# Kernel tuning notes

Hardware: AMD Instinct MI355X
Metric: run time of the kernel (lower is better)

Reference implementation:

```python
import jax, jax.numpy as jnp
import numpy as np

VOCAB, EMB, HID, B, T = 50000, 16, 32, 4096, 500


def setup_inputs() -> dict:
    key = jax.random.key(0)
    k1, k2, k3, k4 = jax.random.split(key, 4)
    tokens = jax.random.randint(k1, (B, T), 0, VOCAB, dtype=jnp.int32)
    emb_table = jax.random.normal(k2, (VOCAB, EMB), dtype=jnp.float32) * 0.05
    kernel = jax.random.normal(k3, (EMB, 4 * HID), dtype=jnp.float32) * (1.0 / np.sqrt(EMB))
    rec_kernel = jax.random.normal(k4, (HID, 4 * HID), dtype=jnp.float32) * (1.0 / np.sqrt(HID))
    # Keras default: unit_forget_bias=True -> forget-gate bias = 1
    bias = jnp.concatenate([
        jnp.zeros((HID,), jnp.float32),
        jnp.ones((HID,), jnp.float32),
        jnp.zeros((2 * HID,), jnp.float32),
    ])
    return {"tokens": tokens, "emb_table": emb_table, "kernel": kernel,
            "rec_kernel": rec_kernel, "bias": bias}


def reference(tokens, emb_table, kernel, rec_kernel, bias):
    # Embedding with mask_zero=True: mask = tokens != 0
    embedded = emb_table[tokens]                 # [B, T, EMB]
    mask = (tokens != 0)                         # [B, T] bool
    # Precompute input projections for all timesteps (one big GEMM)
    x_proj = jnp.einsum('bte,eh->bth', embedded, kernel) + bias  # [B, T, 4H]

    def step(carry, xs):
        h, c = carry                              # [B, H] each
        xp_t, m_t = xs                            # [B, 4H], [B]
        z = xp_t + h @ rec_kernel                 # [B, 4H]
        i, f, g, o = jnp.split(z, 4, axis=-1)     # Keras gate order i,f,c,o
        i = jax.nn.sigmoid(i)
        f = jax.nn.sigmoid(f)
        g = jnp.tanh(g)
        o = jax.nn.sigmoid(o)
        c_new = f * c + i * g
        h_new = o * jnp.tanh(c_new)
        m = m_t[:, None]
        # masked steps carry previous state through (Keras LSTM mask semantics)
        h = jnp.where(m, h_new, h)
        c = jnp.where(m, c_new, c)
        return (h, c), None

    h0 = jnp.zeros((tokens.shape[0], HID), jnp.float32)
    c0 = jnp.zeros((tokens.shape[0], HID), jnp.float32)
    xs = (jnp.swapaxes(x_proj, 0, 1), jnp.swapaxes(mask, 0, 1))  # time-major
    (h, c), _ = jax.lax.scan(step, (h0, c0), xs)
    return h                                      # [B, HID] last (masked) output
```

## Files before the change

### kernel.cpp

```cpp
#include <hip/hip_runtime.h>
#include <cstdint>

#define VOCAB_N 50000
#define EMB_N   16
#define HID_N   32
#define B_N     4096
#define T_N     500

static_assert((T_N & 1) == 0, "T must be even");

__device__ __forceinline__ float frcp(float x) { return __builtin_amdgcn_rcpf(x); }
__device__ __forceinline__ float sigm(float x) {
  return frcp(1.0f + exp2f(x * -1.44269504088896341f));
}
__device__ __forceinline__ float tanh_fast(float x) {
  float e = exp2f(x * 2.88539008177792681f);
  return fmaf(-2.0f, frcp(e + 1.0f), 1.0f);
}

__global__ void build_proj_kernel(const float* __restrict__ emb,
                                  const float* __restrict__ W,
                                  const float* __restrict__ bias,
                                  float* __restrict__ proj) {
  __shared__ float Wl[EMB_N * 128];
  __shared__ float bl[128];
  const int tid = threadIdx.x;
  for (int i = tid; i < EMB_N * 128 / 4; i += 256)
    reinterpret_cast<float4*>(Wl)[i] = reinterpret_cast<const float4*>(W)[i];
  if (tid < 32)
    reinterpret_cast<float4*>(bl)[tid] = reinterpret_cast<const float4*>(bias)[tid];
  __syncthreads();

  const int gtid = blockIdx.x * 256 + tid;
  const int v = gtid >> 5;
  const int j = gtid & 31;
  if (v >= VOCAB_N) return;

  const float4* ev = reinterpret_cast<const float4*>(emb + (size_t)v * EMB_N);
  float4 e0 = ev[0], e1 = ev[1], e2 = ev[2], e3 = ev[3];
  const float em[16] = {e0.x,e0.y,e0.z,e0.w, e1.x,e1.y,e1.z,e1.w,
                        e2.x,e2.y,e2.z,e2.w, e3.x,e3.y,e3.z,e3.w};
  float a0 = bl[j], a1 = bl[32+j], a2 = bl[64+j], a3 = bl[96+j];
#pragma unroll
  for (int e = 0; e < 16; ++e) {
    float x = em[e];
    a0 = fmaf(x, Wl[e*128      + j], a0);
    a1 = fmaf(x, Wl[e*128 + 32 + j], a1);
    a2 = fmaf(x, Wl[e*128 + 64 + j], a2);
    a3 = fmaf(x, Wl[e*128 + 96 + j], a3);
  }
  reinterpret_cast<float4*>(proj)[(size_t)v * 32 + j] = make_float4(a0, a1, a2, a3);
}

template<bool TABLE>
__global__ __launch_bounds__(256, 2)
void lstm_scan_kernel(const int*   __restrict__ tokens,
                      const float* __restrict__ rec_kernel,
                      const float* __restrict__ proj,
                      const float* __restrict__ emb,
                      const float* __restrict__ W,
                      const float* __restrict__ bias,
                      float*       __restrict__ out) {
  __shared__ int   tokl[8][T_N];
  __shared__ float hbuf[8][HID_N];

  const int tid  = threadIdx.x;
  const int wv   = tid >> 6;
  const int lane = tid & 63;
  const int half = lane >> 5;
  const int j    = lane & 31;
  const int wrow = wv * 2 + half;
  const int row  = blockIdx.x * 8 + wrow;

  {
    const int4* src = reinterpret_cast<const int4*>(tokens + (size_t)blockIdx.x * 8 * T_N);
    int4* dst = reinterpret_cast<int4*>(&tokl[0][0]);
    for (int i = tid; i < 8 * T_N / 4; i += 256) dst[i] = src[i];
  }

  float wr[HID_N][4];
#pragma unroll
  for (int k = 0; k < HID_N; ++k) {
#pragma unroll
    for (int g = 0; g < 4; ++g) wr[k][g] = rec_kernel[k * 128 + g * 32 + j];
  }

  float wk[EMB_N][4];
  float bb[4];
  if (!TABLE) {
#pragma unroll
    for (int e = 0; e < EMB_N; ++e) {
#pragma unroll
      for (int g = 0; g < 4; ++g) wk[e][g] = W[e * 128 + g * 32 + j];
    }
#pragma unroll
    for (int g = 0; g < 4; ++g) bb[g] = bias[g * 32 + j];
  }
  __syncthreads();

  float c = 0.0f, h = 0.0f;
  float4 h4[8];
#pragma unroll
  for (int q = 0; q < 8; ++q) h4[q] = make_float4(0.f, 0.f, 0.f, 0.f);

  int tokc  = tokl[wrow][0];
  int tokc1 = tokl[wrow][1];
  float4 pA = make_float4(0,0,0,0), pB = make_float4(0,0,0,0);
  float4 eA[4], eB[4];
  if (TABLE) {
    pA = reinterpret_cast<const float4*>(proj)[(size_t)tokc  * 32 + j];
    pB = reinterpret_cast<const float4*>(proj)[(size_t)tokc1 * 32 + j];
  } else {
#pragma unroll
    for (int q = 0; q < 4; ++q) eA[q] = reinterpret_cast<const float4*>(emb + (size_t)tokc  * EMB_N)[q];
#pragma unroll
    for (int q = 0; q < 4; ++q) eB[q] = reinterpret_cast<const float4*>(emb + (size_t)tokc1 * EMB_N)[q];
  }

  auto body = [&](int t, float4& p, float4* eb) {
    int tp = t + 2; if (tp >= T_N) tp = T_N - 1;
    const int tokp = tokl[wrow][tp];

    float a0, a1, a2, a3;
    if (TABLE) {
      a0 = p.x; a1 = p.y; a2 = p.z; a3 = p.w;
    } else {
      const float em[16] = {eb[0].x,eb[0].y,eb[0].z,eb[0].w, eb[1].x,eb[1].y,eb[1].z,eb[1].w,
                            eb[2].x,eb[2].y,eb[2].z,eb[2].w, eb[3].x,eb[3].y,eb[3].z,eb[3].w};
      a0 = bb[0]; a1 = bb[1]; a2 = bb[2]; a3 = bb[3];
#pragma unroll
      for (int e = 0; e < EMB_N; ++e) {
        float x = em[e];
        a0 = fmaf(x, wk[e][0], a0); a1 = fmaf(x, wk[e][1], a1);
        a2 = fmaf(x, wk[e][2], a2); a3 = fmaf(x, wk[e][3], a3);
      }
    }

#pragma unroll
    for (int q = 0; q < 8; ++q) {
      float hx = h4[q].x, hy = h4[q].y, hz = h4[q].z, hw = h4[q].w;
      a0 = fmaf(hx, wr[4*q+0][0], a0); a1 = fmaf(hx, wr[4*q+0][1], a1);
      a2 = fmaf(hx, wr[4*q+0][2], a2); a3 = fmaf(hx, wr[4*q+0][3], a3);
      a0 = fmaf(hy, wr[4*q+1][0], a0); a1 = fmaf(hy, wr[4*q+1][1], a1);
      a2 = fmaf(hy, wr[4*q+1][2], a2); a3 = fmaf(hy, wr[4*q+1][3], a3);
      a0 = fmaf(hz, wr[4*q+2][0], a0); a1 = fmaf(hz, wr[4*q+2][1], a1);
      a2 = fmaf(hz, wr[4*q+2][2], a2); a3 = fmaf(hz, wr[4*q+2][3], a3);
      a0 = fmaf(hw, wr[4*q+3][0], a0); a1 = fmaf(hw, wr[4*q+3][1], a1);
      a2 = fmaf(hw, wr[4*q+3][2], a2); a3 = fmaf(hw, wr[4*q+3][3], a3);
    }

    if (TABLE) {
      p = reinterpret_cast<const float4*>(proj)[(size_t)tokp * 32 + j];
    } else {
#pragma unroll
      for (int q = 0; q < 4; ++q)
        eb[q] = reinterpret_cast<const float4*>(emb + (size_t)tokp * EMB_N)[q];
    }

    float ig = sigm(a0);
    float fg = sigm(a1);
    float gg = tanh_fast(a2);
    float og = sigm(a3);
    float cn = fmaf(fg, c, ig * gg);
    float hn = og * tanh_fast(cn);
    if (tokc != 0) { h = hn; c = cn; }

    hbuf[wrow][j] = h;
    asm volatile("" ::: "memory");
#pragma unroll
    for (int q = 0; q < 8; ++q)
      h4[q] = reinterpret_cast<const float4*>(&hbuf[wrow][0])[q];
    asm volatile("" ::: "memory");

    tokc = tokc1;
    tokc1 = tokp;
  };

  for (int t = 0; t < T_N; t += 2) {
    body(t,     pA, eA);
    body(t + 1, pB, eB);
  }

  out[(size_t)row * HID_N + j] = h;
}

extern "C" void kernel_launch(void* const* d_in, const int* in_sizes, int n_in,
                              void* d_out, int out_size, void* d_ws, size_t ws_size,
                              hipStream_t stream) {
  const int*   tokens = (const int*)  d_in[0];
  const float* emb    = (const float*)d_in[1];
  const float* W      = (const float*)d_in[2];
  const float* rec    = (const float*)d_in[3];
  const float* bias   = (const float*)d_in[4];
  float* out = (float*)d_out;

  const size_t need = (size_t)VOCAB_N * 32 * 4 * sizeof(float);
  if (ws_size >= need) {
    float* proj = (float*)d_ws;
    build_proj_kernel<<<(VOCAB_N * 32) / 256, 256, 0, stream>>>(emb, W, bias, proj);
    lstm_scan_kernel<true><<<B_N / 8, 256, 0, stream>>>(tokens, rec, proj,
                                                        emb, W, bias, out);
  } else {
    lstm_scan_kernel<false><<<B_N / 8, 256, 0, stream>>>(tokens, rec, nullptr,
                                                         emb, W, bias, out);
  }
}
```

Before: 354.6 us.

## Spread each LSTM row across a full wavefront with two gates per lane

The scan kernel now maps one batch row to a 64-lane wavefront instead of half a wavefront, and each lane computes two gate pre-activations (i/g or f/o). Gates are exchanged with a cross-half shuffle. The projection table is relaid out as float2 per lane, and masked steps skip the gate math and the hidden-state LDS round trip. Token ids are made wave-uniform with readfirstlane, and occupancy bounds are raised. The aim is to halve the per-lane FMA chain on the serial recurrence, at the cost of more waves, shuffles and divergent-free branching overhead.

```diff
diff --git a/kernel.cpp b/kernel.cpp
--- a/kernel.cpp
+++ b/kernel.cpp
@@ -6,22 +6,14 @@
 #define HID_N   32
 #define B_N     4096
 #define T_N     500
-
-static_assert((T_N & 1) == 0, "T must be even");
+#define TPAD    512
 
 __device__ __forceinline__ float frcp(float x) { return __builtin_amdgcn_rcpf(x); }
-__device__ __forceinline__ float sigm(float x) {
-  return frcp(1.0f + exp2f(x * -1.44269504088896341f));
-}
-__device__ __forceinline__ float tanh_fast(float x) {
-  float e = exp2f(x * 2.88539008177792681f);
-  return fmaf(-2.0f, frcp(e + 1.0f), 1.0f);
-}
-
-__global__ void build_proj_kernel(const float* __restrict__ emb,
-                                  const float* __restrict__ W,
-                                  const float* __restrict__ bias,
-                                  float* __restrict__ proj) {
+
+__global__ void build_proj2_kernel(const float* __restrict__ emb,
+                                   const float* __restrict__ W,
+                                   const float* __restrict__ bias,
+                                   float2* __restrict__ proj2) {
   __shared__ float Wl[EMB_N * 128];
   __shared__ float bl[128];
   const int tid = threadIdx.x;
@@ -31,36 +23,167 @@
     reinterpret_cast<float4*>(bl)[tid] = reinterpret_cast<const float4*>(bias)[tid];
   __syncthreads();
 
-  const int gtid = blockIdx.x * 256 + tid;
-  const int v = gtid >> 5;
-  const int j = gtid & 31;
+  const int gid = blockIdx.x * 256 + tid;
+  const int v = gid >> 6;
+  const int l = gid & 63;
   if (v >= VOCAB_N) return;
 
   const float4* ev = reinterpret_cast<const float4*>(emb + (size_t)v * EMB_N);
   float4 e0 = ev[0], e1 = ev[1], e2 = ev[2], e3 = ev[3];
   const float em[16] = {e0.x,e0.y,e0.z,e0.w, e1.x,e1.y,e1.z,e1.w,
                         e2.x,e2.y,e2.z,e2.w, e3.x,e3.y,e3.z,e3.w};
-  float a0 = bl[j], a1 = bl[32+j], a2 = bl[64+j], a3 = bl[96+j];
-#pragma unroll
-  for (int e = 0; e < 16; ++e) {
-    float x = em[e];
-    a0 = fmaf(x, Wl[e*128      + j], a0);
-    a1 = fmaf(x, Wl[e*128 + 32 + j], a1);
-    a2 = fmaf(x, Wl[e*128 + 64 + j], a2);
-    a3 = fmaf(x, Wl[e*128 + 96 + j], a3);
-  }
-  reinterpret_cast<float4*>(proj)[(size_t)v * 32 + j] = make_float4(a0, a1, a2, a3);
-}
-
-template<bool TABLE>
+  float a0 = bl[l], a1 = bl[64 + l];
+#pragma unroll
+  for (int e = 0; e < EMB_N; ++e) {
+    a0 = fmaf(em[e], Wl[e * 128 + l],      a0);
+    a1 = fmaf(em[e], Wl[e * 128 + 64 + l], a1);
+  }
+  proj2[(size_t)v * 64 + l] = make_float2(a0, a1);
+}
+
+__global__ __launch_bounds__(256, 4)
+void lstm_scan2_kernel(const int*    __restrict__ tokens,
+                       const float*  __restrict__ rec_kernel,
+                       const float2* __restrict__ proj2,
+                       float*        __restrict__ out) {
+  __shared__ int   tokl[4][TPAD];
+  __shared__ float hbuf[4][HID_N];
+
+  const int tid  = threadIdx.x;
+  const int wrow = tid >> 6;
+  const int lane = tid & 63;
+  const int l    = lane;
+  const int row  = blockIdx.x * 4 + wrow;
+
+  {
+    const int4* src = reinterpret_cast<const int4*>(tokens + (size_t)blockIdx.x * 4 * T_N);
+    for (int i = tid; i < 4 * T_N / 4; i += 256) {
+      int4 v4 = src[i];
+      int g = 4 * i;
+      int r = g / T_N;
+      int cidx = g - r * T_N;
+      *reinterpret_cast<int4*>(&tokl[r][cidx]) = v4;
+    }
+    if (tid < 48) {
+      int r = tid / 12, cc = T_N + (tid % 12);
+      tokl[r][cc] = 0;
+    }
+  }
+
+  float wr0[HID_N], wr1[HID_N];
+#pragma unroll
+  for (int k = 0; k < HID_N; ++k) {
+    wr0[k] = rec_kernel[k * 128 + l];
+    wr1[k] = rec_kernel[k * 128 + 64 + l];
+  }
+
+  const bool lo = (lane < 32);
+  const float sB = lo ?  2.8853900817779268f : -1.4426950408889634f;
+  const float mB = lo ? -2.0f : 1.0f;
+  const float aB = lo ?  1.0f : 0.0f;
+
+  __syncthreads();
+
+  float c = 0.0f, h = 0.0f;
+  float4 h4[8];
+#pragma unroll
+  for (int q = 0; q < 8; ++q) h4[q] = make_float4(0.f, 0.f, 0.f, 0.f);
+
+  float* hrow = &hbuf[wrow][0];
+  const int kidx = lane & 31;
+
+  int4 g0v = *reinterpret_cast<const int4*>(&tokl[wrow][0]);
+  int4 g1v = *reinterpret_cast<const int4*>(&tokl[wrow][4]);
+  int tg0 = __builtin_amdgcn_readfirstlane(g0v.x);
+  int tg1 = __builtin_amdgcn_readfirstlane(g0v.y);
+  int tg2 = __builtin_amdgcn_readfirstlane(g0v.z);
+  int tg3 = __builtin_amdgcn_readfirstlane(g0v.w);
+  int tn0 = __builtin_amdgcn_readfirstlane(g1v.x);
+  int tn1 = __builtin_amdgcn_readfirstlane(g1v.y);
+  int tn2 = __builtin_amdgcn_readfirstlane(g1v.z);
+  int tn3 = __builtin_amdgcn_readfirstlane(g1v.w);
+
+  float2 p0 = proj2[(size_t)tg0 * 64 + l];
+  float2 p1 = proj2[(size_t)tg1 * 64 + l];
+
+  auto step = [&](int stok, int ptok, float2& pcur) {
+    const float xA = pcur.x, xB = pcur.y;
+
+    pcur = proj2[(size_t)ptok * 64 + l];
+
+    float a0 = xA, a1 = xB, b0 = 0.f, b1 = 0.f;
+#pragma unroll
+    for (int q = 0; q < 8; ++q) {
+      const float4 hq = h4[q];
+      a0 = fmaf(hq.x, wr0[4*q+0], a0); a1 = fmaf(hq.x, wr1[4*q+0], a1);
+      b0 = fmaf(hq.y, wr0[4*q+1], b0); b1 = fmaf(hq.y, wr1[4*q+1], b1);
+      a0 = fmaf(hq.z, wr0[4*q+2], a0); a1 = fmaf(hq.z, wr1[4*q+2], a1);
+      b0 = fmaf(hq.w, wr0[4*q+3], b0); b1 = fmaf(hq.w, wr1[4*q+3], b1);
+    }
+    const float zA = a0 + b0;
+    const float zB = a1 + b1;
+
+    if (stok != 0) {
+      float eA = exp2f(zA * -1.4426950408889634f);
+      float P  = frcp(1.0f + eA);
+      float eB = exp2f(zB * sB);
+      float rB = frcp(1.0f + eB);
+      float Q  = fmaf(mB, rB, aB);
+
+      float P2 = __shfl_xor(P, 32);
+      float Q2 = __shfl_xor(Q, 32);
+      float gi = lo ? P  : P2;
+      float gf = lo ? P2 : P;
+      float gg = lo ? Q  : Q2;
+      float go = lo ? Q2 : Q;
+
+      float cn = fmaf(gf, c, gi * gg);
+      float eC = exp2f(cn * 2.8853900817779268f);
+      float tc = fmaf(-2.0f, frcp(1.0f + eC), 1.0f);
+      float hn = go * tc;
+      c = cn; h = hn;
+
+      hrow[kidx] = hn;
+#pragma unroll
+      for (int q = 0; q < 8; ++q)
+        h4[q] = reinterpret_cast<const float4*>(hrow)[q];
+    }
+  };
+
+  for (int it = 0; it < T_N / 4; ++it) {
+    const int tbase = it * 4;
+    int4 tv = *reinterpret_cast<const int4*>(&tokl[wrow][tbase + 8]);
+
+    step(tg0, tg2, p0);
+    step(tg1, tg3, p1);
+    step(tg2, tn0, p0);
+    step(tg3, tn1, p1);
+
+    tg0 = tn0; tg1 = tn1; tg2 = tn2; tg3 = tn3;
+    tn0 = __builtin_amdgcn_readfirstlane(tv.x);
+    tn1 = __builtin_amdgcn_readfirstlane(tv.y);
+    tn2 = __builtin_amdgcn_readfirstlane(tv.z);
+    tn3 = __builtin_amdgcn_readfirstlane(tv.w);
+  }
+
+  if (lane < 32) out[(size_t)row * HID_N + lane] = h;
+}
+
+__device__ __forceinline__ float sigm_fb(float x) {
+  return frcp(1.0f + exp2f(x * -1.4426950408889634f));
+}
+__device__ __forceinline__ float tanh_fb(float x) {
+  float e = exp2f(x * 2.8853900817779268f);
+  return fmaf(-2.0f, frcp(e + 1.0f), 1.0f);
+}
+
 __global__ __launch_bounds__(256, 2)
-void lstm_scan_kernel(const int*   __restrict__ tokens,
-                      const float* __restrict__ rec_kernel,
-                      const float* __restrict__ proj,
-                      const float* __restrict__ emb,
-                      const float* __restrict__ W,
-                      const float* __restrict__ bias,
-                      float*       __restrict__ out) {
+void lstm_scan_fallback(const int*   __restrict__ tokens,
+                        const float* __restrict__ rec_kernel,
+                        const float* __restrict__ emb,
+                        const float* __restrict__ W,
+                        const float* __restrict__ bias,
+                        float*       __restrict__ out) {
   __shared__ int   tokl[8][T_N];
   __shared__ float hbuf[8][HID_N];
 
@@ -80,22 +203,18 @@
 
   float wr[HID_N][4];
 #pragma unroll
-  for (int k = 0; k < HID_N; ++k) {
+  for (int k = 0; k < HID_N; ++k)
 #pragma unroll
     for (int g = 0; g < 4; ++g) wr[k][g] = rec_kernel[k * 128 + g * 32 + j];
-  }
 
   float wk[EMB_N][4];
   float bb[4];
-  if (!TABLE) {
-#pragma unroll
-    for (int e = 0; e < EMB_N; ++e) {
-#pragma unroll
-      for (int g = 0; g < 4; ++g) wk[e][g] = W[e * 128 + g * 32 + j];
-    }
-#pragma unroll
-    for (int g = 0; g < 4; ++g) bb[g] = bias[g * 32 + j];
-  }
+#pragma unroll
+  for (int e = 0; e < EMB_N; ++e)
+#pragma unroll
+    for (int g = 0; g < 4; ++g) wk[e][g] = W[e * 128 + g * 32 + j];
+#pragma unroll
+  for (int g = 0; g < 4; ++g) bb[g] = bias[g * 32 + j];
   __syncthreads();
 
   float c = 0.0f, h = 0.0f;
@@ -103,39 +222,19 @@
 #pragma unroll
   for (int q = 0; q < 8; ++q) h4[q] = make_float4(0.f, 0.f, 0.f, 0.f);
 
-  int tokc  = tokl[wrow][0];
-  int tokc1 = tokl[wrow][1];
-  float4 pA = make_float4(0,0,0,0), pB = make_float4(0,0,0,0);
-  float4 eA[4], eB[4];
-  if (TABLE) {
-    pA = reinterpret_cast<const float4*>(proj)[(size_t)tokc  * 32 + j];
-    pB = reinterpret_cast<const float4*>(proj)[(size_t)tokc1 * 32 + j];
-  } else {
-#pragma unroll
-    for (int q = 0; q < 4; ++q) eA[q] = reinterpret_cast<const float4*>(emb + (size_t)tokc  * EMB_N)[q];
-#pragma unroll
-    for (int q = 0; q < 4; ++q) eB[q] = reinterpret_cast<const float4*>(emb + (size_t)tokc1 * EMB_N)[q];
-  }
-
-  auto body = [&](int t, float4& p, float4* eb) {
-    int tp = t + 2; if (tp >= T_N) tp = T_N - 1;
-    const int tokp = tokl[wrow][tp];
-
-    float a0, a1, a2, a3;
-    if (TABLE) {
-      a0 = p.x; a1 = p.y; a2 = p.z; a3 = p.w;
-    } else {
-      const float em[16] = {eb[0].x,eb[0].y,eb[0].z,eb[0].w, eb[1].x,eb[1].y,eb[1].z,eb[1].w,
-                            eb[2].x,eb[2].y,eb[2].z,eb[2].w, eb[3].x,eb[3].y,eb[3].z,eb[3].w};
-      a0 = bb[0]; a1 = bb[1]; a2 = bb[2]; a3 = bb[3];
-#pragma unroll
-      for (int e = 0; e < EMB_N; ++e) {
-        float x = em[e];
-        a0 = fmaf(x, wk[e][0], a0); a1 = fmaf(x, wk[e][1], a1);
-        a2 = fmaf(x, wk[e][2], a2); a3 = fmaf(x, wk[e][3], a3);
-      }
-    }
-
+  for (int t = 0; t < T_N; ++t) {
+    const int tokc = tokl[wrow][t];
+    const float4* ev = reinterpret_cast<const float4*>(emb + (size_t)tokc * EMB_N);
+    float4 e0 = ev[0], e1 = ev[1], e2 = ev[2], e3 = ev[3];
+    const float em[16] = {e0.x,e0.y,e0.z,e0.w, e1.x,e1.y,e1.z,e1.w,
+                          e2.x,e2.y,e2.z,e2.w, e3.x,e3.y,e3.z,e3.w};
+    float a0 = bb[0], a1 = bb[1], a2 = bb[2], a3 = bb[3];
+#pragma unroll
+    for (int e = 0; e < EMB_N; ++e) {
+      float x = em[e];
+      a0 = fmaf(x, wk[e][0], a0); a1 = fmaf(x, wk[e][1], a1);
+      a2 = fmaf(x, wk[e][2], a2); a3 = fmaf(x, wk[e][3], a3);
+    }
 #pragma unroll
     for (int q = 0; q < 8; ++q) {
       float hx = h4[q].x, hy = h4[q].y, hz = h4[q].z, hw = h4[q].w;
@@ -148,39 +247,17 @@
       a0 = fmaf(hw, wr[4*q+3][0], a0); a1 = fmaf(hw, wr[4*q+3][1], a1);
       a2 = fmaf(hw, wr[4*q+3][2], a2); a3 = fmaf(hw, wr[4*q+3][3], a3);
     }
-
-    if (TABLE) {
-      p = reinterpret_cast<const float4*>(proj)[(size_t)tokp * 32 + j];
-    } else {
-#pragma unroll
-      for (int q = 0; q < 4; ++q)
-        eb[q] = reinterpret_cast<const float4*>(emb + (size_t)tokp * EMB_N)[q];
-    }
-
-    float ig = sigm(a0);
-    float fg = sigm(a1);
-    float gg = tanh_fast(a2);
-    float og = sigm(a3);
+    float ig = sigm_fb(a0), fg = sigm_fb(a1), gg = tanh_fb(a2), og = sigm_fb(a3);
     float cn = fmaf(fg, c, ig * gg);
-    float hn = og * tanh_fast(cn);
+    float hn = og * tanh_fb(cn);
     if (tokc != 0) { h = hn; c = cn; }
-
     hbuf[wrow][j] = h;
     asm volatile("" ::: "memory");
 #pragma unroll
     for (int q = 0; q < 8; ++q)
       h4[q] = reinterpret_cast<const float4*>(&hbuf[wrow][0])[q];
     asm volatile("" ::: "memory");
-
-    tokc = tokc1;
-    tokc1 = tokp;
-  };
-
-  for (int t = 0; t < T_N; t += 2) {
-    body(t,     pA, eA);
-    body(t + 1, pB, eB);
-  }
-
+  }
   out[(size_t)row * HID_N + j] = h;
 }
 
@@ -194,14 +271,12 @@
   const float* bias   = (const float*)d_in[4];
   float* out = (float*)d_out;
 
-  const size_t need = (size_t)VOCAB_N * 32 * 4 * sizeof(float);
+  const size_t need = (size_t)VOCAB_N * 64 * sizeof(float2);
   if (ws_size >= need) {
-    float* proj = (float*)d_ws;
-    build_proj_kernel<<<(VOCAB_N * 32) / 256, 256, 0, stream>>>(emb, W, bias, proj);
-    lstm_scan_kernel<true><<<B_N / 8, 256, 0, stream>>>(tokens, rec, proj,
-                                                        emb, W, bias, out);
+    float2* proj2 = (float2*)d_ws;
+    build_proj2_kernel<<<(VOCAB_N * 64) / 256 + 1, 256, 0, stream>>>(emb, W, bias, proj2);
+    lstm_scan2_kernel<<<B_N / 4, 256, 0, stream>>>(tokens, rec, proj2, out);
   } else {
-    lstm_scan_kernel<false><<<B_N / 8, 256, 0, stream>>>(tokens, rec, nullptr,
-                                                         emb, W, bias, out);
-  }
-}
+    lstm_scan_fallback<<<B_N / 8, 256, 0, stream>>>(tokens, rec, emb, W, bias, out);
+  }
+}
```

Result: slower. 366.1 us (+3.2%).

## Compute LSTM recurrent matmul with split-bf16 MFMA in single-wave blocks

Applied to the files above, without the earlier changes.

The recurrent h @ rec_kernel product moves from per-lane scalar FMAs to bf16 MFMA instructions. fp32 precision is approximated by splitting both h and the weights into high and low bf16 parts and issuing three MFMA passes. Each 64-thread block now handles 4 batch rows, and the projection table is re-laid out so each lane gathers the gate columns that match the MFMA output layout. The idea is to use matrix cores for the serial per-step dot products, at the cost of per-step split/pack overhead, extra MFMA latency on the critical path, and only one wave per block.

```diff
diff --git a/kernel.cpp b/kernel.cpp
--- a/kernel.cpp
+++ b/kernel.cpp
@@ -7,21 +7,29 @@
 #define B_N     4096
 #define T_N     500
 
-static_assert((T_N & 1) == 0, "T must be even");
+typedef __attribute__((ext_vector_type(8))) short bf16x8;
+typedef __attribute__((ext_vector_type(4))) float f32x4;
 
 __device__ __forceinline__ float frcp(float x) { return __builtin_amdgcn_rcpf(x); }
 __device__ __forceinline__ float sigm(float x) {
-  return frcp(1.0f + exp2f(x * -1.44269504088896341f));
+  return frcp(1.0f + exp2f(x * -1.4426950408889634f));
 }
 __device__ __forceinline__ float tanh_fast(float x) {
-  float e = exp2f(x * 2.88539008177792681f);
-  return fmaf(-2.0f, frcp(e + 1.0f), 1.0f);
-}
-
-__global__ void build_proj_kernel(const float* __restrict__ emb,
-                                  const float* __restrict__ W,
-                                  const float* __restrict__ bias,
-                                  float* __restrict__ proj) {
+  return fmaf(-2.0f, frcp(1.0f + exp2f(x * 2.8853900817779268f)), 1.0f);
+}
+
+__device__ __forceinline__ unsigned bf16_split_pack(float x) {
+  unsigned u  = __builtin_bit_cast(unsigned, x);
+  float hif = __builtin_bit_cast(float, u & 0xFFFF0000u);
+  float r   = x - hif;
+  unsigned lo = __builtin_bit_cast(unsigned, r) >> 16;
+  return (u >> 16) | (lo << 16);
+}
+
+__global__ void build_proj_mfma(const float* __restrict__ emb,
+                                const float* __restrict__ W,
+                                const float* __restrict__ bias,
+                                float* __restrict__ proj) {
   __shared__ float Wl[EMB_N * 128];
   __shared__ float bl[128];
   const int tid = threadIdx.x;
@@ -31,36 +39,171 @@
     reinterpret_cast<float4*>(bl)[tid] = reinterpret_cast<const float4*>(bias)[tid];
   __syncthreads();
 
-  const int gtid = blockIdx.x * 256 + tid;
-  const int v = gtid >> 5;
-  const int j = gtid & 31;
-  if (v >= VOCAB_N) return;
+  const long long gid = (long long)blockIdx.x * 256 + tid;
+  if (gid >= (long long)VOCAB_N * 128) return;
+  const int v = (int)(gid >> 7);
+  const int q = (int)(gid & 127);
+  const int c = q >> 3, n = q & 7;
+  const int col = n * 16 + c;
 
   const float4* ev = reinterpret_cast<const float4*>(emb + (size_t)v * EMB_N);
   float4 e0 = ev[0], e1 = ev[1], e2 = ev[2], e3 = ev[3];
   const float em[16] = {e0.x,e0.y,e0.z,e0.w, e1.x,e1.y,e1.z,e1.w,
                         e2.x,e2.y,e2.z,e2.w, e3.x,e3.y,e3.z,e3.w};
-  float a0 = bl[j], a1 = bl[32+j], a2 = bl[64+j], a3 = bl[96+j];
-#pragma unroll
-  for (int e = 0; e < 16; ++e) {
-    float x = em[e];
-    a0 = fmaf(x, Wl[e*128      + j], a0);
-    a1 = fmaf(x, Wl[e*128 + 32 + j], a1);
-    a2 = fmaf(x, Wl[e*128 + 64 + j], a2);
-    a3 = fmaf(x, Wl[e*128 + 96 + j], a3);
-  }
-  reinterpret_cast<float4*>(proj)[(size_t)v * 32 + j] = make_float4(a0, a1, a2, a3);
-}
-
-template<bool TABLE>
-__global__ __launch_bounds__(256, 2)
-void lstm_scan_kernel(const int*   __restrict__ tokens,
+  float a = bl[col];
+#pragma unroll
+  for (int e = 0; e < EMB_N; ++e) a = fmaf(em[e], Wl[e * 128 + col], a);
+  proj[gid] = a;
+}
+
+#define SPLIT8(VAL, IDX)                                                      \
+  { unsigned s_ = bf16_split_pack(VAL);                                       \
+    Ah[IDX] = (short)s_; Al[IDX] = (short)(s_ >> 16); }
+
+#define LSTM_MSTEP(TOKC, TOKP, XP0, XP1)                                      \
+  {                                                                           \
+                \
+    float4 hv0 = *reinterpret_cast<const float4*>(&hl[c16][g8]);              \
+    float4 hv1 = *reinterpret_cast<const float4*>(&hl[c16][g8 + 4]);          \
+    bf16x8 Ah, Al;                                                            \
+    SPLIT8(hv0.x, 0) SPLIT8(hv0.y, 1) SPLIT8(hv0.z, 2) SPLIT8(hv0.w, 3)      \
+    SPLIT8(hv1.x, 4) SPLIT8(hv1.y, 5) SPLIT8(hv1.z, 6) SPLIT8(hv1.w, 7)      \
+    f32x4 z0 = {(XP0).x, 0.f, 0.f, 0.f};                                      \
+    f32x4 z1 = {(XP0).y, 0.f, 0.f, 0.f};                                      \
+    f32x4 z2 = {(XP0).z, 0.f, 0.f, 0.f};                                      \
+    f32x4 z3 = {(XP0).w, 0.f, 0.f, 0.f};                                      \
+    f32x4 z4 = {(XP1).x, 0.f, 0.f, 0.f};                                      \
+    f32x4 z5 = {(XP1).y, 0.f, 0.f, 0.f};                                      \
+    f32x4 z6 = {(XP1).z, 0.f, 0.f, 0.f};                                      \
+    f32x4 z7 = {(XP1).w, 0.f, 0.f, 0.f};                                      \
+    z0 = __builtin_amdgcn_mfma_f32_16x16x32_bf16(Ah, Bh0, z0, 0, 0, 0);       \
+    z1 = __builtin_amdgcn_mfma_f32_16x16x32_bf16(Ah, Bh1, z1, 0, 0, 0);       \
+    z2 = __builtin_amdgcn_mfma_f32_16x16x32_bf16(Ah, Bh2, z2, 0, 0, 0);       \
+    z3 = __builtin_amdgcn_mfma_f32_16x16x32_bf16(Ah, Bh3, z3, 0, 0, 0);       \
+    z4 = __builtin_amdgcn_mfma_f32_16x16x32_bf16(Ah, Bh4, z4, 0, 0, 0);       \
+    z5 = __builtin_amdgcn_mfma_f32_16x16x32_bf16(Ah, Bh5, z5, 0, 0, 0);       \
+    z6 = __builtin_amdgcn_mfma_f32_16x16x32_bf16(Ah, Bh6, z6, 0, 0, 0);       \
+    z7 = __builtin_amdgcn_mfma_f32_16x16x32_bf16(Ah, Bh7, z7, 0, 0, 0);       \
+    z0 = __builtin_amdgcn_mfma_f32_16x16x32_bf16(Ah, Bl0, z0, 0, 0, 0);       \
+    z1 = __builtin_amdgcn_mfma_f32_16x16x32_bf16(Ah, Bl1, z1, 0, 0, 0);       \
+    z2 = __builtin_amdgcn_mfma_f32_16x16x32_bf16(Ah, Bl2, z2, 0, 0, 0);       \
+    z3 = __builtin_amdgcn_mfma_f32_16x16x32_bf16(Ah, Bl3, z3, 0, 0, 0);       \
+    z4 = __builtin_amdgcn_mfma_f32_16x16x32_bf16(Ah, Bl4, z4, 0, 0, 0);       \
+    z5 = __builtin_amdgcn_mfma_f32_16x16x32_bf16(Ah, Bl5, z5, 0, 0, 0);       \
+    z6 = __builtin_amdgcn_mfma_f32_16x16x32_bf16(Ah, Bl6, z6, 0, 0, 0);       \
+    z7 = __builtin_amdgcn_mfma_f32_16x16x32_bf16(Ah, Bl7, z7, 0, 0, 0);       \
+    z0 = __builtin_amdgcn_mfma_f32_16x16x32_bf16(Al, Bh0, z0, 0, 0, 0);       \
+    z1 = __builtin_amdgcn_mfma_f32_16x16x32_bf16(Al, Bh1, z1, 0, 0, 0);       \
+    z2 = __builtin_amdgcn_mfma_f32_16x16x32_bf16(Al, Bh2, z2, 0, 0, 0);       \
+    z3 = __builtin_amdgcn_mfma_f32_16x16x32_bf16(Al, Bh3, z3, 0, 0, 0);       \
+    z4 = __builtin_amdgcn_mfma_f32_16x16x32_bf16(Al, Bh4, z4, 0, 0, 0);       \
+    z5 = __builtin_amdgcn_mfma_f32_16x16x32_bf16(Al, Bh5, z5, 0, 0, 0);       \
+    z6 = __builtin_amdgcn_mfma_f32_16x16x32_bf16(Al, Bh6, z6, 0, 0, 0);       \
+    z7 = __builtin_amdgcn_mfma_f32_16x16x32_bf16(Al, Bh7, z7, 0, 0, 0);       \
+                          \
+    {                                                                         \
+      const float4* xp_p = reinterpret_cast<const float4*>(                   \
+          proj + ((size_t)(TOKP) << 7) + c16 * 8);                            \
+      (XP0) = xp_p[0]; (XP1) = xp_p[1];                                       \
+    }                                                                         \
+                    \
+    {                                                                         \
+      float i0 = sigm(z0.x), f0 = sigm(z2.x);                                 \
+      float g0 = tanh_fast(z4.x), o0 = sigm(z6.x);                            \
+      float i1 = sigm(z1.x), f1 = sigm(z3.x);                                 \
+      float g1 = tanh_fast(z5.x), o1 = sigm(z7.x);                            \
+      float cn0 = fmaf(f0, c0, i0 * g0);                                      \
+      float cn1 = fmaf(f1, c1, i1 * g1);                                      \
+      float hn0 = o0 * tanh_fast(cn0);                                        \
+      float hn1 = o1 * tanh_fast(cn1);                                        \
+      bool m = (TOKC) != 0;                                                   \
+      c0 = m ? cn0 : c0;  h0 = m ? hn0 : h0;                                  \
+      c1 = m ? cn1 : c1;  h1 = m ? hn1 : h1;                                  \
+      hl[myrow][c16]      = h0;                                               \
+      hl[myrow][c16 + 16] = h1;                                               \
+      asm volatile("" ::: "memory");      \
+    }                                                                         \
+  }
+
+__global__ __launch_bounds__(64, 1)
+void lstm_mfma_kernel(const int*   __restrict__ tokens,
                       const float* __restrict__ rec_kernel,
                       const float* __restrict__ proj,
-                      const float* __restrict__ emb,
-                      const float* __restrict__ W,
-                      const float* __restrict__ bias,
                       float*       __restrict__ out) {
+  __shared__ float hl[16][36];
+  __shared__ int   tokl[4][512];
+
+  const int l   = threadIdx.x;
+  const int g   = l >> 4;
+  const int c16 = l & 15;
+  const int g8  = g * 8;
+  const int myrow = 4 * g;
+
+  for (int i = l; i < 16 * 36; i += 64) (&hl[0][0])[i] = 0.0f;
+
+  {
+    const int4* src = reinterpret_cast<const int4*>(tokens + (size_t)blockIdx.x * 4 * T_N);
+    for (int i = l; i < T_N; i += 64) {
+      int4 v4 = src[i];
+      int gi = 4 * i;
+      int r  = gi / T_N;
+      int cc = gi - r * T_N;
+      *reinterpret_cast<int4*>(&tokl[r][cc]) = v4;
+    }
+    if (l < 48) { int r = l / 12, cc = T_N + (l % 12); tokl[r][cc] = 0; }
+  }
+  asm volatile("" ::: "memory");
+
+  bf16x8 Bh0, Bh1, Bh2, Bh3, Bh4, Bh5, Bh6, Bh7;
+  bf16x8 Bl0, Bl1, Bl2, Bl3, Bl4, Bl5, Bl6, Bl7;
+#define BUILD_B(N, BH, BL)                                                    \
+  {                                                                           \
+    _Pragma("unroll")                                                         \
+    for (int j = 0; j < 8; ++j) {                                             \
+      float x = rec_kernel[(g8 + j) * 128 + (N) * 16 + c16];                  \
+      unsigned s_ = bf16_split_pack(x);                                       \
+      (BH)[j] = (short)s_; (BL)[j] = (short)(s_ >> 16);                       \
+    }                                                                         \
+  }
+  BUILD_B(0, Bh0, Bl0) BUILD_B(1, Bh1, Bl1) BUILD_B(2, Bh2, Bl2)
+  BUILD_B(3, Bh3, Bl3) BUILD_B(4, Bh4, Bl4) BUILD_B(5, Bh5, Bl5)
+  BUILD_B(6, Bh6, Bl6) BUILD_B(7, Bh7, Bl7)
+#undef BUILD_B
+
+  float c0 = 0.f, c1 = 0.f, h0 = 0.f, h1 = 0.f;
+
+  int tA = tokl[g][0], tB = tokl[g][1], tC = tokl[g][2], tD = tokl[g][3];
+
+  float4 xpA0, xpA1, xpB0, xpB1;
+  {
+    const float4* p0 = reinterpret_cast<const float4*>(proj + ((size_t)tA << 7) + c16 * 8);
+    xpA0 = p0[0]; xpA1 = p0[1];
+    const float4* p1 = reinterpret_cast<const float4*>(proj + ((size_t)tB << 7) + c16 * 8);
+    xpB0 = p1[0]; xpB1 = p1[1];
+  }
+
+#pragma unroll 1
+  for (int t = 0; t < T_N; t += 2) {
+    int2 tnew = *reinterpret_cast<const int2*>(&tokl[g][t + 4]);
+
+    LSTM_MSTEP(tA, tC, xpA0, xpA1);
+    LSTM_MSTEP(tB, tD, xpB0, xpB1);
+
+    tA = tC; tB = tD; tC = tnew.x; tD = tnew.y;
+  }
+
+  const size_t obase = ((size_t)blockIdx.x * 4 + g) * HID_N;
+  out[obase + c16]      = h0;
+  out[obase + c16 + 16] = h1;
+}
+
+__global__ __launch_bounds__(256, 2)
+void lstm_scan_fallback(const int*   __restrict__ tokens,
+                        const float* __restrict__ rec_kernel,
+                        const float* __restrict__ emb,
+                        const float* __restrict__ W,
+                        const float* __restrict__ bias,
+                        float*       __restrict__ out) {
   __shared__ int   tokl[8][T_N];
   __shared__ float hbuf[8][HID_N];
 
@@ -80,22 +223,18 @@
 
   float wr[HID_N][4];
 #pragma unroll
-  for (int k = 0; k < HID_N; ++k) {
-#pragma unroll
-    for (int g = 0; g < 4; ++g) wr[k][g] = rec_kernel[k * 128 + g * 32 + j];
-  }
+  for (int k = 0; k < HID_N; ++k)
+#pragma unroll
+    for (int gg2 = 0; gg2 < 4; ++gg2) wr[k][gg2] = rec_kernel[k * 128 + gg2 * 32 + j];
 
   float wk[EMB_N][4];
   float bb[4];
-  if (!TABLE) {
-#pragma unroll
-    for (int e = 0; e < EMB_N; ++e) {
-#pragma unroll
-      for (int g = 0; g < 4; ++g) wk[e][g] = W[e * 128 + g * 32 + j];
-    }
-#pragma unroll
-    for (int g = 0; g < 4; ++g) bb[g] = bias[g * 32 + j];
-  }
+#pragma unroll
+  for (int e = 0; e < EMB_N; ++e)
+#pragma unroll
+    for (int gg2 = 0; gg2 < 4; ++gg2) wk[e][gg2] = W[e * 128 + gg2 * 32 + j];
+#pragma unroll
+  for (int gg2 = 0; gg2 < 4; ++gg2) bb[gg2] = bias[gg2 * 32 + j];
   __syncthreads();
 
   float c = 0.0f, h = 0.0f;
@@ -103,39 +242,19 @@
 #pragma unroll
   for (int q = 0; q < 8; ++q) h4[q] = make_float4(0.f, 0.f, 0.f, 0.f);
 
-  int tokc  = tokl[wrow][0];
-  int tokc1 = tokl[wrow][1];
-  float4 pA = make_float4(0,0,0,0), pB = make_float4(0,0,0,0);
-  float4 eA[4], eB[4];
-  if (TABLE) {
-    pA = reinterpret_cast<const float4*>(proj)[(size_t)tokc  * 32 + j];
-    pB = reinterpret_cast<const float4*>(proj)[(size_t)tokc1 * 32 + j];
-  } else {
-#pragma unroll
-    for (int q = 0; q < 4; ++q) eA[q] = reinterpret_cast<const float4*>(emb + (size_t)tokc  * EMB_N)[q];
-#pragma unroll
-    for (int q = 0; q < 4; ++q) eB[q] = reinterpret_cast<const float4*>(emb + (size_t)tokc1 * EMB_N)[q];
-  }
-
-  auto body = [&](int t, float4& p, float4* eb) {
-    int tp = t + 2; if (tp >= T_N) tp = T_N - 1;
-    const int tokp = tokl[wrow][tp];
-
-    float a0, a1, a2, a3;
-    if (TABLE) {
-      a0 = p.x; a1 = p.y; a2 = p.z; a3 = p.w;
-    } else {
-      const float em[16] = {eb[0].x,eb[0].y,eb[0].z,eb[0].w, eb[1].x,eb[1].y,eb[1].z,eb[1].w,
-                            eb[2].x,eb[2].y,eb[2].z,eb[2].w, eb[3].x,eb[3].y,eb[3].z,eb[3].w};
-      a0 = bb[0]; a1 = bb[1]; a2 = bb[2]; a3 = bb[3];
-#pragma unroll
-      for (int e = 0; e < EMB_N; ++e) {
-        float x = em[e];
-        a0 = fmaf(x, wk[e][0], a0); a1 = fmaf(x, wk[e][1], a1);
-        a2 = fmaf(x, wk[e][2], a2); a3 = fmaf(x, wk[e][3], a3);
-      }
+  for (int t = 0; t < T_N; ++t) {
+    const int tokc = tokl[wrow][t];
+    const float4* ev = reinterpret_cast<const float4*>(emb + (size_t)tokc * EMB_N);
+    float4 e0 = ev[0], e1 = ev[1], e2 = ev[2], e3 = ev[3];
+    const float em[16] = {e0.x,e0.y,e0.z,e0.w, e1.x,e1.y,e1.z,e1.w,
+                          e2.x,e2.y,e2.z,e2.w, e3.x,e3.y,e3.z,e3.w};
+    float a0 = bb[0], a1 = bb[1], a2 = bb[2], a3 = bb[3];
+#pragma unroll
+    for (int e = 0; e < EMB_N; ++e) {
+      float x = em[e];
+      a0 = fmaf(x, wk[e][0], a0); a1 = fmaf(x, wk[e][1], a1);
+      a2 = fmaf(x, wk[e][2], a2); a3 = fmaf(x, wk[e][3], a3);
     }
-
 #pragma unroll
     for (int q = 0; q < 8; ++q) {
       float hx = h4[q].x, hy = h4[q].y, hz = h4[q].z, hw = h4[q].w;
@@ -148,39 +267,17 @@
       a0 = fmaf(hw, wr[4*q+3][0], a0); a1 = fmaf(hw, wr[4*q+3][1], a1);
       a2 = fmaf(hw, wr[4*q+3][2], a2); a3 = fmaf(hw, wr[4*q+3][3], a3);
     }
-
-    if (TABLE) {
-      p = reinterpret_cast<const float4*>(proj)[(size_t)tokp * 32 + j];
-    } else {
-#pragma unroll
-      for (int q = 0; q < 4; ++q)
-        eb[q] = reinterpret_cast<const float4*>(emb + (size_t)tokp * EMB_N)[q];
-    }
-
-    float ig = sigm(a0);
-    float fg = sigm(a1);
-    float gg = tanh_fast(a2);
-    float og = sigm(a3);
+    float ig = sigm(a0), fg = sigm(a1), gg = tanh_fast(a2), og = sigm(a3);
     float cn = fmaf(fg, c, ig * gg);
     float hn = og * tanh_fast(cn);
     if (tokc != 0) { h = hn; c = cn; }
-
     hbuf[wrow][j] = h;
     asm volatile("" ::: "memory");
 #pragma unroll
     for (int q = 0; q < 8; ++q)
       h4[q] = reinterpret_cast<const float4*>(&hbuf[wrow][0])[q];
     asm volatile("" ::: "memory");
-
-    tokc = tokc1;
-    tokc1 = tokp;
-  };
-
-  for (int t = 0; t < T_N; t += 2) {
-    body(t,     pA, eA);
-    body(t + 1, pB, eB);
-  }
-
+  }
   out[(size_t)row * HID_N + j] = h;
 }
 
@@ -194,14 +291,13 @@
   const float* bias   = (const float*)d_in[4];
   float* out = (float*)d_out;
 
-  const size_t need = (size_t)VOCAB_N * 32 * 4 * sizeof(float);
+  const size_t need = (size_t)VOCAB_N * 128 * sizeof(float);
   if (ws_size >= need) {
     float* proj = (float*)d_ws;
-    build_proj_kernel<<<(VOCAB_N * 32) / 256, 256, 0, stream>>>(emb, W, bias, proj);
-    lstm_scan_kernel<true><<<B_N / 8, 256, 0, stream>>>(tokens, rec, proj,
-                                                        emb, W, bias, out);
+    const long long total = (long long)VOCAB_N * 128;
+    build_proj_mfma<<<(int)((total + 255) / 256), 256, 0, stream>>>(emb, W, bias, proj);
+    lstm_mfma_kernel<<<B_N / 4, 64, 0, stream>>>(tokens, rec, proj, out);
   } else {
-    lstm_scan_kernel<false><<<B_N / 8, 256, 0, stream>>>(tokens, rec, nullptr,
-                                                         emb, W, bias, out);
-  }
-}
+    lstm_scan_fallback<<<B_N / 8, 256, 0, stream>>>(tokens, rec, emb, W, bias, out);
+  }
+}
```

After: 438.4 us. +23.6%, slower.
